# Optimization experiments

Hardware: AMD Instinct MI355X
Metric: run time of the kernel (lower is better)

Reference implementation:

```python
import jax, jax.numpy as jnp
import numpy as np

N = 2048        # samples per batch
IN = 256        # in_size
OUT = 256       # out_size
T = 128         # num_tasks


def setup_inputs() -> dict:
    key = jax.random.key(0)
    k1, k2, k3 = jax.random.split(key, 3)
    inputs = jax.random.normal(k1, (N, IN), dtype=jnp.float32)
    task_ids = jax.random.randint(k2, (N,), 0, T, dtype=jnp.int64)
    # Task-specific weight table [num_tasks, in_size, out_size],
    # kaiming-style scale 1/sqrt(in_size).
    W = jax.random.normal(k3, (T, IN, OUT), dtype=jnp.float32) / jnp.sqrt(
        jnp.float32(IN)
    )
    return {"inputs": inputs, "task_ids": task_ids, "W": W}


def reference(inputs, task_ids, W):
    # _get_matrices: gather per-sample weight matrix by task id -> [N, in, out]
    mats = W[task_ids]
    # einsum 'ni,nio->no': per-sample matvec
    return jnp.einsum("ni,nio->no", inputs, mats)
```

## Files before the change

### kernel.cpp

```cpp
#include <hip/hip_runtime.h>
#include <hip/hip_bf16.h>


#define NSAMP 2048
#define NTASK 128
#define INSZ  256
#define OUTSZ 256
#define CHUNK 8
#define MAXC  6
#define PF    8

__global__ __launch_bounds__(256, 3)
void TaskSpecificLinear_24910810316924_kernel(
    const float* __restrict__ X,
    const int*   __restrict__ ids32,
    const float* __restrict__ W,
    float*       __restrict__ out)
{
    __shared__ float xt[INSZ * CHUNK];
    __shared__ float pacc[4 * CHUNK * 128];
    __shared__ int   s_list[CHUNK];
    __shared__ int   s_wcnt[4];
    __shared__ int   s_odd;

    const int tid  = threadIdx.x;
    const int t    = blockIdx.x;
    const int c    = blockIdx.y;
    const int lane = tid & 63;
    const int wv   = tid >> 6;

    if (tid == 0) s_odd = 0;
    if (tid < CHUNK) s_list[tid] = -1;
    __syncthreads();

    if (ids32[1 + 8 * tid]) s_odd = 1;
    __syncthreads();
    const bool is64 = (s_odd == 0);

    int match[8];
    if (is64) {
        #pragma unroll
        for (int j = 0; j < 8; ++j)
            match[j] = (((const int2*)ids32)[tid * 8 + j].x == t);
    } else {
        #pragma unroll
        for (int j = 0; j < 8; ++j)
            match[j] = (ids32[tid * 8 + j] == t);
    }

    unsigned long long mask[8];
    int wave_total = 0;
    #pragma unroll
    for (int j = 0; j < 8; ++j) {
        mask[j] = __ballot(match[j]);
        wave_total += __popcll(mask[j]);
    }
    if (lane == 0) s_wcnt[wv] = wave_total;
    __syncthreads();

    const int b0 = s_wcnt[0], b1 = s_wcnt[1], b2 = s_wcnt[2], b3 = s_wcnt[3];
    const int count = b0 + b1 + b2 + b3;
    const int len   = min(CHUNK, count - c * CHUNK);
    if (len <= 0) return;

    {
        int r = (wv > 0 ? b0 : 0) + (wv > 1 ? b1 : 0) + (wv > 2 ? b2 : 0);
        const unsigned long long below = (1ULL << lane) - 1ULL;
        #pragma unroll
        for (int j = 0; j < 8; ++j) {
            if (match[j]) {
                int rank = r + __popcll(mask[j] & below);
                int rr = rank - c * CHUNK;
                if (rr >= 0 && rr < CHUNK)
                    s_list[rr] = tid * 8 + j;
            }
            r += __popcll(mask[j]);
        }
    }
    __syncthreads();

    #pragma unroll
    for (int s = 0; s < CHUNK; ++s) {
        int n = s_list[s];
        float v = 0.f;
        if (n >= 0) v = X[(size_t)n * INSZ + tid];
        xt[tid * CHUNK + s] = v;
    }
    __syncthreads();

    for (int half = 0; half < 2; ++half) {
        const int col0 = half * 128 + lane * 2;
        const float* wp = W + ((size_t)t * INSZ + wv * 64) * OUTSZ + col0;

        float2 acc[CHUNK];
        #pragma unroll
        for (int s = 0; s < CHUNK; ++s) acc[s] = make_float2(0.f, 0.f);

        float2 wbuf[PF];
        #pragma unroll
        for (int k = 0; k < PF; ++k)
            wbuf[k] = *(const float2*)(wp + k * OUTSZ);

        #pragma unroll
        for (int g = 0; g < 64 / PF; ++g) {
            float2 wnext[PF];
            if (g < 64 / PF - 1) {
                #pragma unroll
                for (int k = 0; k < PF; ++k)
                    wnext[k] = *(const float2*)(wp + ((g + 1) * PF + k) * OUTSZ);
            }
            #pragma unroll
            for (int k = 0; k < PF; ++k) {
                const int i = g * PF + k;
                const float2 w2 = wbuf[k];
                const float4 xa = *(const float4*)&xt[(wv * 64 + i) * CHUNK];
                const float4 xb = *(const float4*)&xt[(wv * 64 + i) * CHUNK + 4];
                acc[0].x += xa.x * w2.x; acc[0].y += xa.x * w2.y;
                acc[1].x += xa.y * w2.x; acc[1].y += xa.y * w2.y;
                acc[2].x += xa.z * w2.x; acc[2].y += xa.z * w2.y;
                acc[3].x += xa.w * w2.x; acc[3].y += xa.w * w2.y;
                acc[4].x += xb.x * w2.x; acc[4].y += xb.x * w2.y;
                acc[5].x += xb.y * w2.x; acc[5].y += xb.y * w2.y;
                acc[6].x += xb.z * w2.x; acc[6].y += xb.z * w2.y;
                acc[7].x += xb.w * w2.x; acc[7].y += xb.w * w2.y;
            }
            if (g < 64 / PF - 1) {
                #pragma unroll
                for (int k = 0; k < PF; ++k)
                    wbuf[k] = wnext[k];
            }
        }

        float* pb = &pacc[wv * (CHUNK * 128) + lane * 2];
        #pragma unroll
        for (int s = 0; s < CHUNK; ++s)
            *(float2*)&pb[s * 128] = acc[s];
        __syncthreads();

        {
            const int e = tid * 4;
            float4 v = make_float4(0.f, 0.f, 0.f, 0.f);
            #pragma unroll
            for (int w2i = 0; w2i < 4; ++w2i) {
                const float4 p = *(const float4*)&pacc[w2i * 1024 + e];
                v.x += p.x; v.y += p.y; v.z += p.z; v.w += p.w;
            }
            const int s  = e >> 7;
            const int lc = e & 127;
            const int n  = s_list[s];
            if (n >= 0)
                *(float4*)&out[(size_t)n * OUTSZ + half * 128 + lc] = v;
        }
        __syncthreads();
    }
}

extern "C" void kernel_launch(void* const* d_in, const int* in_sizes, int n_in,
                              void* d_out, int out_size, void* d_ws, size_t ws_size,
                              hipStream_t stream) {
    const float* X   = (const float*)d_in[0];
    const int*   ids = (const int*)d_in[1];
    const float* W   = (const float*)d_in[2];
    float*       out = (float*)d_out;

    dim3 grid(NTASK, MAXC, 1);
    dim3 block(256, 1, 1);
    TaskSpecificLinear_24910810316924_kernel<<<grid, block, 0, stream>>>(X, ids, W, out);
}
```

Before: 87.05 us.

## Replace fixed task-by-chunk grid with histogram-driven persistent job list

Every block now builds a per-task histogram of task ids in shared memory with atomics, scans chunk counts, and forms a compact job list of (task, chunk) pairs. A fixed grid of 768 blocks then strides over the jobs, so no blocks are launched for empty chunks and the old fixed cap of six chunks per task no longer applies. Jobs are grouped into 8 residue classes by a transposed task order, likely to spread tasks across XCDs for L2 locality. In exchange, every block repeats the histogram and scan, which adds redundant prologue work and extra barriers.

```diff
diff --git a/kernel.cpp b/kernel.cpp
--- a/kernel.cpp
+++ b/kernel.cpp
@@ -7,7 +7,7 @@
 #define INSZ  256
 #define OUTSZ 256
 #define CHUNK 8
-#define MAXC  6
+#define NBLK  768
 #define PF    8
 
 __global__ __launch_bounds__(256, 3)
@@ -19,139 +19,186 @@
 {
     __shared__ float xt[INSZ * CHUNK];
     __shared__ float pacc[4 * CHUNK * 128];
+    __shared__ int   cnt[NTASK];
+    __shared__ int   scanbuf[NTASK];
+    __shared__ int   jt[NTASK * 3];
     __shared__ int   s_list[CHUNK];
     __shared__ int   s_wcnt[4];
     __shared__ int   s_odd;
 
     const int tid  = threadIdx.x;
-    const int t    = blockIdx.x;
-    const int c    = blockIdx.y;
+    const int bid  = blockIdx.x;
     const int lane = tid & 63;
     const int wv   = tid >> 6;
 
     if (tid == 0) s_odd = 0;
-    if (tid < CHUNK) s_list[tid] = -1;
+    if (tid < NTASK) cnt[tid] = 0;
     __syncthreads();
 
     if (ids32[1 + 8 * tid]) s_odd = 1;
     __syncthreads();
     const bool is64 = (s_odd == 0);
 
-    int match[8];
+    int myid[8];
     if (is64) {
         #pragma unroll
         for (int j = 0; j < 8; ++j)
-            match[j] = (((const int2*)ids32)[tid * 8 + j].x == t);
+            myid[j] = ((const int2*)ids32)[tid * 8 + j].x;
     } else {
         #pragma unroll
         for (int j = 0; j < 8; ++j)
-            match[j] = (ids32[tid * 8 + j] == t);
-    }
-
-    unsigned long long mask[8];
-    int wave_total = 0;
+            myid[j] = ids32[tid * 8 + j];
+    }
+
     #pragma unroll
-    for (int j = 0; j < 8; ++j) {
-        mask[j] = __ballot(match[j]);
-        wave_total += __popcll(mask[j]);
-    }
-    if (lane == 0) s_wcnt[wv] = wave_total;
-    __syncthreads();
-
-    const int b0 = s_wcnt[0], b1 = s_wcnt[1], b2 = s_wcnt[2], b3 = s_wcnt[3];
-    const int count = b0 + b1 + b2 + b3;
-    const int len   = min(CHUNK, count - c * CHUNK);
-    if (len <= 0) return;
-
-    {
-        int r = (wv > 0 ? b0 : 0) + (wv > 1 ? b1 : 0) + (wv > 2 ? b2 : 0);
-        const unsigned long long below = (1ULL << lane) - 1ULL;
-        #pragma unroll
-        for (int j = 0; j < 8; ++j) {
-            if (match[j]) {
-                int rank = r + __popcll(mask[j] & below);
-                int rr = rank - c * CHUNK;
-                if (rr >= 0 && rr < CHUNK)
-                    s_list[rr] = tid * 8 + j;
-            }
-            r += __popcll(mask[j]);
-        }
-    }
-    __syncthreads();
-
+    for (int j = 0; j < 8; ++j)
+        atomicAdd(&cnt[myid[j]], 1);
+    __syncthreads();
+
+    if (tid < NTASK) {
+        const int tp = ((tid & 15) << 3) | (tid >> 4);
+        scanbuf[tid] = (cnt[tp] + CHUNK - 1) >> 3;
+    }
+    __syncthreads();
     #pragma unroll
-    for (int s = 0; s < CHUNK; ++s) {
-        int n = s_list[s];
-        float v = 0.f;
-        if (n >= 0) v = X[(size_t)n * INSZ + tid];
-        xt[tid * CHUNK + s] = v;
-    }
-    __syncthreads();
-
-    for (int half = 0; half < 2; ++half) {
-        const int col0 = half * 128 + lane * 2;
-        const float* wp = W + ((size_t)t * INSZ + wv * 64) * OUTSZ + col0;
-
-        float2 acc[CHUNK];
-        #pragma unroll
-        for (int s = 0; s < CHUNK; ++s) acc[s] = make_float2(0.f, 0.f);
-
-        float2 wbuf[PF];
-        #pragma unroll
-        for (int k = 0; k < PF; ++k)
-            wbuf[k] = *(const float2*)(wp + k * OUTSZ);
-
-        #pragma unroll
-        for (int g = 0; g < 64 / PF; ++g) {
-            float2 wnext[PF];
-            if (g < 64 / PF - 1) {
+    for (int off = 1; off < NTASK; off <<= 1) {
+        int v = 0;
+        if (tid < NTASK) {
+            v = scanbuf[tid];
+            if (tid >= off) v += scanbuf[tid - off];
+        }
+        __syncthreads();
+        if (tid < NTASK) scanbuf[tid] = v;
+        __syncthreads();
+    }
+
+    if (tid < NTASK) {
+        const int tp  = ((tid & 15) << 3) | (tid >> 4);
+        const int nch = (cnt[tp] + CHUNK - 1) >> 3;
+        const int base = scanbuf[tid] - nch;
+        for (int c = 0; c < nch; ++c)
+            jt[base + c] = tp | (c << 8);
+    }
+    __syncthreads();
+
+    const int r = bid & 7;
+    const int q = bid >> 3;
+    const int resbase = (r == 0) ? 0 : scanbuf[r * 16 - 1];
+    const int resend  = scanbuf[r * 16 + 15];
+
+    for (int j = resbase + q; j < resend; j += 96) {
+        const int d = jt[j];
+        const int t = d & 255;
+        const int c = d >> 8;
+
+        int match[8];
+        #pragma unroll
+        for (int k = 0; k < 8; ++k) match[k] = (myid[k] == t);
+
+        unsigned long long mask[8];
+        int wave_total = 0;
+        #pragma unroll
+        for (int k = 0; k < 8; ++k) {
+            mask[k] = __ballot(match[k]);
+            wave_total += __popcll(mask[k]);
+        }
+        if (lane == 0) s_wcnt[wv] = wave_total;
+        if (tid < CHUNK) s_list[tid] = -1;
+        __syncthreads();
+
+        const int b0 = s_wcnt[0], b1 = s_wcnt[1], b2 = s_wcnt[2];
+        {
+            int rk = (wv > 0 ? b0 : 0) + (wv > 1 ? b1 : 0) + (wv > 2 ? b2 : 0);
+            const unsigned long long below = (1ULL << lane) - 1ULL;
+            #pragma unroll
+            for (int k = 0; k < 8; ++k) {
+                if (match[k]) {
+                    int rank = rk + __popcll(mask[k] & below);
+                    int rr = rank - c * CHUNK;
+                    if (rr >= 0 && rr < CHUNK)
+                        s_list[rr] = tid * 8 + k;
+                }
+                rk += __popcll(mask[k]);
+            }
+        }
+        __syncthreads();
+
+        #pragma unroll
+        for (int s = 0; s < CHUNK; ++s) {
+            const int n = s_list[s];
+            float v = 0.f;
+            if (n >= 0) v = X[(size_t)n * INSZ + tid];
+            xt[tid * CHUNK + s] = v;
+        }
+        __syncthreads();
+
+        for (int half = 0; half < 2; ++half) {
+            const int col0 = half * 128 + lane * 2;
+            const float* wp = W + ((size_t)t * INSZ + wv * 64) * OUTSZ + col0;
+
+            float2 acc[CHUNK];
+            #pragma unroll
+            for (int s = 0; s < CHUNK; ++s) acc[s] = make_float2(0.f, 0.f);
+
+            float2 wbuf[PF];
+            #pragma unroll
+            for (int k = 0; k < PF; ++k)
+                wbuf[k] = *(const float2*)(wp + k * OUTSZ);
+
+            #pragma unroll
+            for (int g = 0; g < 64 / PF; ++g) {
+                float2 wnext[PF];
+                if (g < 64 / PF - 1) {
+                    #pragma unroll
+                    for (int k = 0; k < PF; ++k)
+                        wnext[k] = *(const float2*)(wp + ((g + 1) * PF + k) * OUTSZ);
+                }
                 #pragma unroll
-                for (int k = 0; k < PF; ++k)
-                    wnext[k] = *(const float2*)(wp + ((g + 1) * PF + k) * OUTSZ);
-            }
-            #pragma unroll
-            for (int k = 0; k < PF; ++k) {
-                const int i = g * PF + k;
-                const float2 w2 = wbuf[k];
-                const float4 xa = *(const float4*)&xt[(wv * 64 + i) * CHUNK];
-                const float4 xb = *(const float4*)&xt[(wv * 64 + i) * CHUNK + 4];
-                acc[0].x += xa.x * w2.x; acc[0].y += xa.x * w2.y;
-                acc[1].x += xa.y * w2.x; acc[1].y += xa.y * w2.y;
-                acc[2].x += xa.z * w2.x; acc[2].y += xa.z * w2.y;
-                acc[3].x += xa.w * w2.x; acc[3].y += xa.w * w2.y;
-                acc[4].x += xb.x * w2.x; acc[4].y += xb.x * w2.y;
-                acc[5].x += xb.y * w2.x; acc[5].y += xb.y * w2.y;
-                acc[6].x += xb.z * w2.x; acc[6].y += xb.z * w2.y;
-                acc[7].x += xb.w * w2.x; acc[7].y += xb.w * w2.y;
-            }
-            if (g < 64 / PF - 1) {
+                for (int k = 0; k < PF; ++k) {
+                    const int i = g * PF + k;
+                    const float2 w2 = wbuf[k];
+                    const float4 xa = *(const float4*)&xt[(wv * 64 + i) * CHUNK];
+                    const float4 xb = *(const float4*)&xt[(wv * 64 + i) * CHUNK + 4];
+                    acc[0].x += xa.x * w2.x; acc[0].y += xa.x * w2.y;
+                    acc[1].x += xa.y * w2.x; acc[1].y += xa.y * w2.y;
+                    acc[2].x += xa.z * w2.x; acc[2].y += xa.z * w2.y;
+                    acc[3].x += xa.w * w2.x; acc[3].y += xa.w * w2.y;
+                    acc[4].x += xb.x * w2.x; acc[4].y += xb.x * w2.y;
+                    acc[5].x += xb.y * w2.x; acc[5].y += xb.y * w2.y;
+                    acc[6].x += xb.z * w2.x; acc[6].y += xb.z * w2.y;
+                    acc[7].x += xb.w * w2.x; acc[7].y += xb.w * w2.y;
+                }
+                if (g < 64 / PF - 1) {
+                    #pragma unroll
+                    for (int k = 0; k < PF; ++k)
+                        wbuf[k] = wnext[k];
+                }
+            }
+
+            {
+                float* pb = &pacc[wv * (CHUNK * 128) + lane * 2];
                 #pragma unroll
-                for (int k = 0; k < PF; ++k)
-                    wbuf[k] = wnext[k];
-            }
-        }
-
-        float* pb = &pacc[wv * (CHUNK * 128) + lane * 2];
-        #pragma unroll
-        for (int s = 0; s < CHUNK; ++s)
-            *(float2*)&pb[s * 128] = acc[s];
-        __syncthreads();
-
-        {
-            const int e = tid * 4;
-            float4 v = make_float4(0.f, 0.f, 0.f, 0.f);
-            #pragma unroll
-            for (int w2i = 0; w2i < 4; ++w2i) {
-                const float4 p = *(const float4*)&pacc[w2i * 1024 + e];
-                v.x += p.x; v.y += p.y; v.z += p.z; v.w += p.w;
-            }
-            const int s  = e >> 7;
-            const int lc = e & 127;
-            const int n  = s_list[s];
-            if (n >= 0)
-                *(float4*)&out[(size_t)n * OUTSZ + half * 128 + lc] = v;
-        }
-        __syncthreads();
+                for (int s = 0; s < CHUNK; ++s)
+                    *(float2*)&pb[s * 128] = acc[s];
+            }
+            __syncthreads();
+
+            {
+                const int e = tid * 4;
+                float4 v = make_float4(0.f, 0.f, 0.f, 0.f);
+                #pragma unroll
+                for (int qq = 0; qq < 4; ++qq) {
+                    const float4 p = *(const float4*)&pacc[qq * 1024 + e];
+                    v.x += p.x; v.y += p.y; v.z += p.z; v.w += p.w;
+                }
+                const int s  = e >> 7;
+                const int lc = e & 127;
+                const int n  = s_list[s];
+                if (n >= 0)
+                    *(float4*)&out[(size_t)n * OUTSZ + half * 128 + lc] = v;
+            }
+            __syncthreads();
+        }
     }
 }
 
@@ -163,7 +210,7 @@
     const float* W   = (const float*)d_in[2];
     float*       out = (float*)d_out;
 
-    dim3 grid(NTASK, MAXC, 1);
+    dim3 grid(NBLK, 1, 1);
     dim3 block(256, 1, 1);
     TaskSpecificLinear_24910810316924_kernel<<<grid, block, 0, stream>>>(X, ids, W, out);
 }
```

After: 88.19 us. About the same (+1.3%).
